# Kernel tuning notes

Measured on AMD Instinct MI355X. Metric: run time of the kernel, lower is better.

## Reference

```python
import jax, jax.numpy as jnp
import numpy as np

D_MODEL = 1024
N_HEADS = 16
D_HEAD = D_MODEL // N_HEADS


def setup_inputs() -> dict:
    key = jax.random.key(0)
    k_x, k_qkv, k_proj = jax.random.split(key, 3)
    x = jax.random.normal(k_x, (4, 2048, D_MODEL), dtype=jnp.float32)
    # nn.Linear(d_model, 3*d_model, bias=False): weight shape [3*d_model, d_model]
    scale = 1.0 / np.sqrt(D_MODEL)
    W_qkv = jax.random.uniform(k_qkv, (3 * D_MODEL, D_MODEL), dtype=jnp.float32, minval=-scale, maxval=scale)
    W_proj = jax.random.uniform(k_proj, (D_MODEL, D_MODEL), dtype=jnp.float32, minval=-scale, maxval=scale)
    return {"x": x, "W_qkv": W_qkv, "W_proj": W_proj}


def reference(x, W_qkv, W_proj):
    B, T, C = x.shape
    qkv = jnp.einsum('btc,fc->btf', x, W_qkv)  # [B,T,3C]
    q, k, v = jnp.split(qkv, 3, axis=-1)
    # [B,T,H,Dh] -> [B,H,T,Dh]
    q = q.reshape(B, T, N_HEADS, D_HEAD).transpose(0, 2, 1, 3)
    k = k.reshape(B, T, N_HEADS, D_HEAD).transpose(0, 2, 1, 3)
    v = v.reshape(B, T, N_HEADS, D_HEAD).transpose(0, 2, 1, 3)
    att = jnp.einsum('bhqd,bhkd->bhqk', q, k) / jnp.sqrt(jnp.float32(D_HEAD))
    att = jax.nn.softmax(att, axis=-1)
    y = jnp.einsum('bhqk,bhkd->bhqd', att, v)
    y = y.transpose(0, 2, 1, 3).reshape(B, T, C)
    return jnp.einsum('btc,oc->bto', y, W_proj)
```

## Files before the change

kernel.cpp:

```cpp
#include <hip/hip_runtime.h>
#include <stdint.h>
#include <stddef.h>

#define SEQ   2048
#define NH    16
#define DH    64
#define DM    1024
#define NTOK  8192

typedef unsigned short u16;
typedef unsigned int u32;
typedef short bf16x8 __attribute__((ext_vector_type(8)));
typedef short bf16x4 __attribute__((ext_vector_type(4)));
typedef float f32x4  __attribute__((ext_vector_type(4)));
typedef unsigned short u16x4 __attribute__((ext_vector_type(4)));
typedef unsigned short u16x8 __attribute__((ext_vector_type(8)));
typedef unsigned int u32x4 __attribute__((ext_vector_type(4)));

#define QSCALE 0.18033688011112042f

#define WAIT_VM12 0x0F7C
#define WAIT_VM2  0x0F72
#define WAIT_VM0  0x0F70

__device__ __forceinline__ u16 f2bf(float f) {
  union { float f; unsigned u; } v; v.f = f;
  return (u16)((v.u + 0x7FFFu + ((v.u >> 16) & 1u)) >> 16);
}

__device__ __forceinline__ void gload_lds16(const void* g, void* l) {
  __builtin_amdgcn_global_load_lds(
      (const __attribute__((address_space(1))) void*)g,
      (__attribute__((address_space(3))) void*)l, 16, 0, 0);
}

__device__ __forceinline__ bf16x8 cat44(bf16x4 a, bf16x4 b) {
  bf16x8 r;
  r[0] = a[0]; r[1] = a[1]; r[2] = a[2]; r[3] = a[3];
  r[4] = b[0]; r[5] = b[1]; r[6] = b[2]; r[7] = b[3];
  return r;
}

__global__ __launch_bounds__(256) void cast_kernel(const float* __restrict__ src,
                                                   u16* __restrict__ dst, int n4) {
  int i = blockIdx.x * 256 + threadIdx.x;
  if (i < n4) {
    const float4 f = ((const float4*)src)[i];
    u16x4 o;
    o.x = f2bf(f.x); o.y = f2bf(f.y); o.z = f2bf(f.z); o.w = f2bf(f.w);
    ((u16x4*)dst)[i] = o;
  }
}

__global__ __launch_bounds__(256) void pack_b(const float* __restrict__ W,
                                              u16* __restrict__ Bp, int NS) {
  const int chunk = blockIdx.x * 256 + threadIdx.x;
  const int lane = chunk & 63, blk = chunk >> 6;
  const int c = blk / NS, s = blk % NS;
  const int n = s * 16 + (lane & 15);
  const int k0 = c * 32 + (lane >> 4) * 8;
  const float4 f0 = *(const float4*)&W[(size_t)n * DM + k0];
  const float4 f1 = *(const float4*)&W[(size_t)n * DM + k0 + 4];
  u16x8 o;
  o[0] = f2bf(f0.x); o[1] = f2bf(f0.y); o[2] = f2bf(f0.z); o[3] = f2bf(f0.w);
  o[4] = f2bf(f1.x); o[5] = f2bf(f1.y); o[6] = f2bf(f1.z); o[7] = f2bf(f1.w);
  *(u16x8*)&Bp[(size_t)chunk * 8] = o;
}

template <int EPI>
__global__ __launch_bounds__(256) void gemm_flat(
    const u16* __restrict__ A, const u16* __restrict__ Bp, int NS, int N_,
    u16* __restrict__ Qo, u16* __restrict__ Ko, u16* __restrict__ Vto,
    float* __restrict__ Co) {
  __shared__ __align__(16) u16 sA[2][128 * 64];
  const int tid = threadIdx.x;
  const int wave = tid >> 6, lane = tid & 63;
  const int l16 = lane & 15, quad = lane >> 4;
  const int sw = l16 & 7;
  const int wm = (wave >> 1) * 64, wn = (wave & 1) * 64;
  const int nbx = (int)gridDim.x;
  const int id = (int)(blockIdx.y * nbx + blockIdx.x);
  const int cpx = (int)(gridDim.x * gridDim.y) >> 3;
  const int wid = (id & 7) * cpx + (id >> 3);
  const int row0 = (wid / nbx) * 128, col0 = (wid % nbx) * 128;
  const int ck0 = ((quad ^ sw) << 3);
  const int ck1 = (((quad + 4) ^ sw) << 3);
  const int scol = (col0 + wn) >> 4;
  const u16* bpw = Bp + (size_t)lane * 8;

  f32x4 acc[4][4];
  for (int a = 0; a < 4; ++a)
    for (int b = 0; b < 4; ++b) acc[a][b] = (f32x4){0.f, 0.f, 0.f, 0.f};

  bf16x8 bfr[2][2][4];

  for (int j = 0; j < 4; ++j) {
    const int li = j * 256 + tid;
    const int r = li >> 3;
    const int cs = (((li & 7) ^ (r & 7)) << 3);
    gload_lds16(A + (size_t)(row0 + r) * DM + cs, (char*)sA[0] + li * 16);
  }
  for (int kk = 0; kk < 2; ++kk) {
    const u16* bb = bpw + ((size_t)kk * NS + scol) * 512;
    for (int i = 0; i < 4; ++i)
      bfr[0][kk][i] = *(const bf16x8*)(bb + i * 512);
  }

#pragma unroll 2
  for (int t = 0; t < 16; ++t) {
    const int cur = t & 1;
    const int tn = (t + 1) & 15;
    const int k1 = tn << 6;
    for (int j = 0; j < 4; ++j) {
      const int li = j * 256 + tid;
      const int r = li >> 3;
      const int cs = (((li & 7) ^ (r & 7)) << 3);
      gload_lds16(A + (size_t)(row0 + r) * DM + k1 + cs, (char*)sA[cur ^ 1] + li * 16);
    }
    for (int kk = 0; kk < 2; ++kk) {
      const u16* bb = bpw + ((size_t)(tn * 2 + kk) * NS + scol) * 512;
      for (int i = 0; i < 4; ++i)
        bfr[cur ^ 1][kk][i] = *(const bf16x8*)(bb + i * 512);
    }
    __builtin_amdgcn_s_waitcnt(WAIT_VM12);
    __builtin_amdgcn_s_barrier();
    const u16* sa = sA[cur];
    for (int kk = 0; kk < 2; ++kk) {
      const int cko = kk ? ck1 : ck0;
      bf16x8 af[4];
      for (int i = 0; i < 4; ++i)
        af[i] = *(const bf16x8*)&sa[(wm + i * 16 + l16) * 64 + cko];
      for (int mi = 0; mi < 4; ++mi)
        for (int ni = 0; ni < 4; ++ni)
          acc[mi][ni] = __builtin_amdgcn_mfma_f32_16x16x32_bf16(
              af[mi], bfr[cur][kk][ni], acc[mi][ni], 0, 0, 0);
    }
    __builtin_amdgcn_s_barrier();
  }
  __builtin_amdgcn_s_waitcnt(WAIT_VM0);

  if (EPI == 0) {
    const int which = col0 >> 10;
    for (int mi = 0; mi < 4; ++mi)
      for (int ni = 0; ni < 4; ++ni) {
        const int rowb = row0 + wm + mi * 16 + quad * 4;
        const int col = col0 + wn + ni * 16 + l16;
        const int b = rowb >> 11, t = rowb & (SEQ - 1);
        const int c = col & (DM - 1);
        const int h = c >> 6, d = c & 63;
        const size_t bh = (size_t)b * NH + h;
        if (which == 2) {
          u16x4 pk;
          pk.x = f2bf(acc[mi][ni][0]); pk.y = f2bf(acc[mi][ni][1]);
          pk.z = f2bf(acc[mi][ni][2]); pk.w = f2bf(acc[mi][ni][3]);
          *(u16x4*)&Vto[(bh * DH + d) * SEQ + t] = pk;
        } else {
          for (int r = 0; r < 4; ++r) {
            const float v = acc[mi][ni][r];
            if (which == 0) Qo[(bh * SEQ + t + r) * DH + d] = f2bf(v * QSCALE);
            else            Ko[(bh * SEQ + t + r) * DH + d] = f2bf(v);
          }
        }
      }
  } else {
    for (int mi = 0; mi < 4; ++mi)
      for (int ni = 0; ni < 4; ++ni)
        for (int r = 0; r < 4; ++r) {
          const int row = row0 + wm + mi * 16 + quad * 4 + r;
          const int col = col0 + wn + ni * 16 + l16;
          Co[(size_t)row * N_ + col] = acc[mi][ni][r];
        }
  }
}

__global__ __launch_bounds__(512, 4) void flash_attn(
    const u16* __restrict__ Q, const u16* __restrict__ Kk,
    const u16* __restrict__ Vt, u16* __restrict__ Y) {
  __shared__ __align__(16) u16 sK[2][64 * 64];
  __shared__ __align__(16) u16 sV[2][64 * 64];
  const int tid = threadIdx.x, wave = tid >> 6, lane = tid & 63;
  const int l16 = lane & 15, quad = lane >> 4;
  const int sw = l16 & 7;
  const int ck0 = ((quad ^ sw) << 3);
  const int ck1 = (((quad + 4) ^ sw) << 3);
  const int rloc = tid >> 3;
  const int cs = (((tid & 7) ^ (rloc & 7)) << 3);
  const int id = (int)(blockIdx.y * 8 + blockIdx.x);
  const int wid = (id & 7) * 64 + (id >> 3);
  const int bh = wid >> 3;
  const int q0 = (wid & 7) * 256 + wave * 32;
  const size_t qkBase = (size_t)bh * SEQ * DH;
  const size_t vtBase = (size_t)bh * DH * SEQ;

  const int q2 = quad >> 1, q1o = (quad & 1) << 2;
  const int vA0 = (((q2 + 0) ^ sw) << 3) + q1o;
  const int vB0 = (((q2 + 2) ^ sw) << 3) + q1o;
  const int vA1 = (((q2 + 4) ^ sw) << 3) + q1o;
  const int vB1 = (((q2 + 6) ^ sw) << 3) + q1o;

  bf16x8 qf[2][2];
  for (int ms = 0; ms < 2; ++ms) {
    const u16* qrow = Q + qkBase + (size_t)(q0 + ms * 16 + l16) * DH;
    qf[ms][0] = *(const bf16x8*)(qrow + quad * 8);
    qf[ms][1] = *(const bf16x8*)(qrow + 32 + quad * 8);
  }

  bf16x8 onesf;
  for (int i = 0; i < 8; ++i) onesf[i] = (short)0x3F80;

  f32x4 o[2][4];
  f32x4 osum[2];
  for (int a = 0; a < 2; ++a) {
    osum[a] = (f32x4){0.f, 0.f, 0.f, 0.f};
    for (int b = 0; b < 4; ++b) o[a][b] = (f32x4){0.f, 0.f, 0.f, 0.f};
  }

  gload_lds16(Kk + qkBase + (size_t)rloc * DH + cs, (char*)sK[0] + tid * 16);
  gload_lds16(Vt + vtBase + (size_t)rloc * SEQ + cs, (char*)sV[0] + tid * 16);
  for (int t = 0; t < 32; ++t) {
    const int cur = t & 1;
    const int kt1 = ((t + 1) & 31) * 64;
    gload_lds16(Kk + qkBase + (size_t)(kt1 + rloc) * DH + cs, (char*)sK[cur ^ 1] + tid * 16);
    gload_lds16(Vt + vtBase + (size_t)rloc * SEQ + kt1 + cs, (char*)sV[cur ^ 1] + tid * 16);
    __builtin_amdgcn_s_waitcnt(WAIT_VM2);
    __builtin_amdgcn_s_barrier();
    const u16* sk = sK[cur];
    const u16* sv = sV[cur];

    u32x4 pw[2][2];
#pragma unroll
    for (int nt = 0; nt < 4; ++nt) {
      const bf16x8 kf0 = *(const bf16x8*)&sk[(nt * 16 + l16) * 64 + ck0];
      const bf16x8 kf1 = *(const bf16x8*)&sk[(nt * 16 + l16) * 64 + ck1];
#pragma unroll
      for (int ms = 0; ms < 2; ++ms) {
        f32x4 st = (f32x4){0.f, 0.f, 0.f, 0.f};
        __builtin_amdgcn_s_setprio(1);
        st = __builtin_amdgcn_mfma_f32_16x16x32_bf16(kf0, qf[ms][0], st, 0, 0, 0);
        st = __builtin_amdgcn_mfma_f32_16x16x32_bf16(kf1, qf[ms][1], st, 0, 0, 0);
        __builtin_amdgcn_s_setprio(0);
        const u32 u0 = __builtin_bit_cast(u32, __builtin_amdgcn_exp2f(st[0]));
        const u32 u1 = __builtin_bit_cast(u32, __builtin_amdgcn_exp2f(st[1]));
        const u32 u2 = __builtin_bit_cast(u32, __builtin_amdgcn_exp2f(st[2]));
        const u32 u3 = __builtin_bit_cast(u32, __builtin_amdgcn_exp2f(st[3]));
        pw[ms][nt >> 1][(nt & 1) * 2]     = __builtin_amdgcn_perm(u1, u0, 0x07060302u);
        pw[ms][nt >> 1][(nt & 1) * 2 + 1] = __builtin_amdgcn_perm(u3, u2, 0x07060302u);
      }
    }

    __builtin_amdgcn_s_setprio(1);
#pragma unroll
    for (int ms = 0; ms < 2; ++ms) {
      osum[ms] = __builtin_amdgcn_mfma_f32_16x16x32_bf16(
          __builtin_bit_cast(bf16x8, pw[ms][0]), onesf, osum[ms], 0, 0, 0);
      osum[ms] = __builtin_amdgcn_mfma_f32_16x16x32_bf16(
          __builtin_bit_cast(bf16x8, pw[ms][1]), onesf, osum[ms], 0, 0, 0);
    }

#pragma unroll
    for (int ds = 0; ds < 4; ++ds) {
      const int rb = (ds * 16 + l16) * 64;
      const bf16x8 vf0 = cat44(*(const bf16x4*)&sv[rb + vA0],
                               *(const bf16x4*)&sv[rb + vB0]);
      const bf16x8 vf1 = cat44(*(const bf16x4*)&sv[rb + vA1],
                               *(const bf16x4*)&sv[rb + vB1]);
#pragma unroll
      for (int ms = 0; ms < 2; ++ms) {
        o[ms][ds] = __builtin_amdgcn_mfma_f32_16x16x32_bf16(
            __builtin_bit_cast(bf16x8, pw[ms][0]), vf0, o[ms][ds], 0, 0, 0);
        o[ms][ds] = __builtin_amdgcn_mfma_f32_16x16x32_bf16(
            __builtin_bit_cast(bf16x8, pw[ms][1]), vf1, o[ms][ds], 0, 0, 0);
      }
    }
    __builtin_amdgcn_s_setprio(0);
    __builtin_amdgcn_s_barrier();
  }
  __builtin_amdgcn_s_waitcnt(WAIT_VM0);

  float rl[2][4];
  for (int ms = 0; ms < 2; ++ms)
    for (int r = 0; r < 4; ++r)
      rl[ms][r] = __frcp_rn(osum[ms][r]);

  const int b = bh >> 4, h = bh & (NH - 1);
  for (int ms = 0; ms < 2; ++ms)
    for (int ds = 0; ds < 4; ++ds)
      for (int r = 0; r < 4; ++r) {
        const int t = q0 + ms * 16 + quad * 4 + r;
        const int d = ds * 16 + l16;
        Y[((size_t)(b * SEQ + t)) * DM + h * DH + d] = f2bf(o[ms][ds][r] * rl[ms][r]);
      }
}

extern "C" void kernel_launch(void* const* d_in, const int* in_sizes, int n_in,
                              void* d_out, int out_size, void* d_ws, size_t ws_size,
                              hipStream_t stream) {
  const float* x     = (const float*)d_in[0];
  const float* Wqkv  = (const float*)d_in[1];
  const float* Wproj = (const float*)d_in[2];
  float* out = (float*)d_out;

  u16* xb     = (u16*)d_ws;
  u16* bpQkv  = xb + (size_t)NTOK * DM;
  u16* bpProj = bpQkv + (size_t)3 * DM * DM;
  u16* Qb  = bpProj + (size_t)DM * DM;
  u16* Kb  = Qb + (size_t)NTOK * DM;
  u16* Vtb = Kb + (size_t)NTOK * DM;
  u16* Yb  = Vtb + (size_t)NTOK * DM;

  {
    int n4 = NTOK * DM / 4;
    cast_kernel<<<(n4 + 255) / 256, 256, 0, stream>>>(x, xb, n4);
    pack_b<<<3 * DM * DM / 8 / 256, 256, 0, stream>>>(Wqkv, bpQkv, 3 * DM / 16);
    pack_b<<<DM * DM / 8 / 256, 256, 0, stream>>>(Wproj, bpProj, DM / 16);
  }

  gemm_flat<0><<<dim3(3 * DM / 128, NTOK / 128), 256, 0, stream>>>(
      xb, bpQkv, 3 * DM / 16, 3 * DM, Qb, Kb, Vtb, nullptr);

  flash_attn<<<dim3(SEQ / 256, 4 * NH), 512, 0, stream>>>(Qb, Kb, Vtb, Yb);

  gemm_flat<1><<<dim3(DM / 128, NTOK / 128), 256, 0, stream>>>(
      Yb, bpProj, DM / 16, DM, nullptr, nullptr, nullptr, out);
}
```

Baseline: 260.0 us.

## Deepen GEMM pipeline to triple-buffered LDS with 256-row tiles and LDS-staged B

Replaces the double-buffered 128x128 GEMM with a 512-thread kernel computing 256x128 tiles. Both A and packed B are staged into LDS through a three-deep ring, so two K-steps are prefetched ahead, and MFMA sections run at raised wave priority. The aim is to hide global-load latency better and share B fragments across more rows. The cost is much more LDS per block (about 144 KB), which limits occupancy, and half as many blocks for the projection GEMM.

```diff
diff --git a/kernel.cpp b/kernel.cpp
--- a/kernel.cpp
+++ b/kernel.cpp
@@ -19,7 +19,7 @@
 
 #define QSCALE 0.18033688011112042f
 
-#define WAIT_VM12 0x0F7C
+#define WAIT_VM6  0x0F76
 #define WAIT_VM2  0x0F72
 #define WAIT_VM0  0x0F70
 
@@ -67,12 +67,15 @@
   *(u16x8*)&Bp[(size_t)chunk * 8] = o;
 }
 
+#define GA_SZ (256 * 64)
+#define GB_SZ (128 * 64)
 template <int EPI>
-__global__ __launch_bounds__(256) void gemm_flat(
+__global__ __launch_bounds__(512, 2) void gemm_deep(
     const u16* __restrict__ A, const u16* __restrict__ Bp, int NS, int N_,
     u16* __restrict__ Qo, u16* __restrict__ Ko, u16* __restrict__ Vto,
     float* __restrict__ Co) {
-  __shared__ __align__(16) u16 sA[2][128 * 64];
+  __shared__ __align__(16) u16 sA[3][GA_SZ];
+  __shared__ __align__(16) u16 sB[3][GB_SZ];
   const int tid = threadIdx.x;
   const int wave = tid >> 6, lane = tid & 63;
   const int l16 = lane & 15, quad = lane >> 4;
@@ -82,62 +85,71 @@
   const int id = (int)(blockIdx.y * nbx + blockIdx.x);
   const int cpx = (int)(gridDim.x * gridDim.y) >> 3;
   const int wid = (id & 7) * cpx + (id >> 3);
-  const int row0 = (wid / nbx) * 128, col0 = (wid % nbx) * 128;
+  const int row0 = (wid / nbx) * 256, col0 = (wid % nbx) * 128;
   const int ck0 = ((quad ^ sw) << 3);
   const int ck1 = (((quad + 4) ^ sw) << 3);
-  const int scol = (col0 + wn) >> 4;
-  const u16* bpw = Bp + (size_t)lane * 8;
+  const int scol0 = col0 >> 4;
+  const int fb0 = wave * 2;
+  const int kkA = fb0 >> 3, sA_ = fb0 & 7;
 
   f32x4 acc[4][4];
   for (int a = 0; a < 4; ++a)
     for (int b = 0; b < 4; ++b) acc[a][b] = (f32x4){0.f, 0.f, 0.f, 0.f};
 
-  bf16x8 bfr[2][2][4];
-
-  for (int j = 0; j < 4; ++j) {
-    const int li = j * 256 + tid;
-    const int r = li >> 3;
-    const int cs = (((li & 7) ^ (r & 7)) << 3);
-    gload_lds16(A + (size_t)(row0 + r) * DM + cs, (char*)sA[0] + li * 16);
-  }
-  for (int kk = 0; kk < 2; ++kk) {
-    const u16* bb = bpw + ((size_t)kk * NS + scol) * 512;
-    for (int i = 0; i < 4; ++i)
-      bfr[0][kk][i] = *(const bf16x8*)(bb + i * 512);
-  }
-
-#pragma unroll 2
+#define STAGE(kt, dA, dB)                                                      \
+  do {                                                                         \
+    for (int j = 0; j < 4; ++j) {                                              \
+      const int li = j * 512 + tid;                                            \
+      const int r = li >> 3;                                                   \
+      const int cs = (((li & 7) ^ (r & 7)) << 3);                              \
+      gload_lds16(A + (size_t)(row0 + r) * DM + ((kt) << 6) + cs,              \
+                  (char*)(dA) + li * 16);                                      \
+    }                                                                          \
+    gload_lds16(Bp + ((size_t)((kt) * 2 + kkA) * NS + scol0 + sA_) * 512 +     \
+                    lane * 8,                                                  \
+                (char*)(dB) + fb0 * 1024);                                     \
+    gload_lds16(Bp + ((size_t)((kt) * 2 + kkA) * NS + scol0 + sA_ + 1) * 512 + \
+                    lane * 8,                                                  \
+                (char*)(dB) + (fb0 + 1) * 1024);                               \
+  } while (0)
+
+  STAGE(0, sA[0], sB[0]);
+  STAGE(1, sA[1], sB[1]);
+  __builtin_amdgcn_s_waitcnt(WAIT_VM6);
+  __builtin_amdgcn_s_barrier();
+
+  int cur = 0;
   for (int t = 0; t < 16; ++t) {
-    const int cur = t & 1;
-    const int tn = (t + 1) & 15;
-    const int k1 = tn << 6;
-    for (int j = 0; j < 4; ++j) {
-      const int li = j * 256 + tid;
-      const int r = li >> 3;
-      const int cs = (((li & 7) ^ (r & 7)) << 3);
-      gload_lds16(A + (size_t)(row0 + r) * DM + k1 + cs, (char*)sA[cur ^ 1] + li * 16);
-    }
-    for (int kk = 0; kk < 2; ++kk) {
-      const u16* bb = bpw + ((size_t)(tn * 2 + kk) * NS + scol) * 512;
-      for (int i = 0; i < 4; ++i)
-        bfr[cur ^ 1][kk][i] = *(const bf16x8*)(bb + i * 512);
-    }
-    __builtin_amdgcn_s_waitcnt(WAIT_VM12);
+    const int tn = (t + 2) & 15;
+    int pre = cur + 2; if (pre >= 3) pre -= 3;
+    STAGE(tn, sA[pre], sB[pre]);
+    const u16* sa = sA[cur];
+    const u16* sb = sB[cur];
+    bf16x8 af0[4], af1[4], bf0[4], bf1[4];
+    for (int mi = 0; mi < 4; ++mi)
+      af0[mi] = *(const bf16x8*)&sa[(wm + mi * 16 + l16) * 64 + ck0];
+    for (int ni = 0; ni < 4; ++ni)
+      bf0[ni] = *(const bf16x8*)&sb[(((wn >> 4) + ni) * 512) + lane * 8];
+    for (int mi = 0; mi < 4; ++mi)
+      af1[mi] = *(const bf16x8*)&sa[(wm + mi * 16 + l16) * 64 + ck1];
+    for (int ni = 0; ni < 4; ++ni)
+      bf1[ni] = *(const bf16x8*)&sb[((8 + (wn >> 4) + ni) * 512) + lane * 8];
+    __builtin_amdgcn_s_setprio(1);
+    for (int mi = 0; mi < 4; ++mi)
+      for (int ni = 0; ni < 4; ++ni)
+        acc[mi][ni] = __builtin_amdgcn_mfma_f32_16x16x32_bf16(
+            af0[mi], bf0[ni], acc[mi][ni], 0, 0, 0);
+    for (int mi = 0; mi < 4; ++mi)
+      for (int ni = 0; ni < 4; ++ni)
+        acc[mi][ni] = __builtin_amdgcn_mfma_f32_16x16x32_bf16(
+            af1[mi], bf1[ni], acc[mi][ni], 0, 0, 0);
+    __builtin_amdgcn_s_setprio(0);
+    __builtin_amdgcn_s_waitcnt(WAIT_VM6);
     __builtin_amdgcn_s_barrier();
-    const u16* sa = sA[cur];
-    for (int kk = 0; kk < 2; ++kk) {
-      const int cko = kk ? ck1 : ck0;
-      bf16x8 af[4];
-      for (int i = 0; i < 4; ++i)
-        af[i] = *(const bf16x8*)&sa[(wm + i * 16 + l16) * 64 + cko];
-      for (int mi = 0; mi < 4; ++mi)
-        for (int ni = 0; ni < 4; ++ni)
-          acc[mi][ni] = __builtin_amdgcn_mfma_f32_16x16x32_bf16(
-              af[mi], bfr[cur][kk][ni], acc[mi][ni], 0, 0, 0);
-    }
-    __builtin_amdgcn_s_barrier();
+    cur = cur + 1 == 3 ? 0 : cur + 1;
   }
   __builtin_amdgcn_s_waitcnt(WAIT_VM0);
+#undef STAGE
 
   if (EPI == 0) {
     const int which = col0 >> 10;
@@ -315,11 +327,11 @@
     pack_b<<<DM * DM / 8 / 256, 256, 0, stream>>>(Wproj, bpProj, DM / 16);
   }
 
-  gemm_flat<0><<<dim3(3 * DM / 128, NTOK / 128), 256, 0, stream>>>(
+  gemm_deep<0><<<dim3(3 * DM / 128, NTOK / 256), 512, 0, stream>>>(
       xb, bpQkv, 3 * DM / 16, 3 * DM, Qb, Kb, Vtb, nullptr);
 
   flash_attn<<<dim3(SEQ / 256, 4 * NH), 512, 0, stream>>>(Qb, Kb, Vtb, Yb);
 
-  gemm_flat<1><<<dim3(DM / 128, NTOK / 128), 256, 0, stream>>>(
+  gemm_deep<1><<<dim3(DM / 128, NTOK / 256), 512, 0, stream>>>(
       Yb, bpProj, DM / 16, DM, nullptr, nullptr, nullptr, out);
 }
```

Result: slower. 266.1 us (+2.3%).
